# Optimization experiments

Hardware: AMD Instinct MI355X
Metric: run time of the kernel (lower is better)

The kernel has to match this reference:

```python
import jax, jax.numpy as jnp
import numpy as np

B, L, D, H = 2, 2048, 1024, 16
DH = D // H
TAU = 0.1


def setup_inputs() -> dict:
    key = jax.random.key(0)
    ks = jax.random.split(key, 12)
    s = 0.02
    return {
        "q_x": jax.random.normal(ks[0], (B, L, D), jnp.float32),
        "k_x": jax.random.normal(ks[1], (B, L, D), jnp.float32),
        "v_x": jax.random.normal(ks[2], (B, L, D), jnp.float32),
        "ec": jax.random.normal(ks[3], (B, L, D), jnp.float32),
        "Wq": jax.random.normal(ks[4], (D, D), jnp.float32) * s,
        "bq": jnp.zeros((D,), jnp.float32),
        "Wk": jax.random.normal(ks[5], (D, D), jnp.float32) * s,
        "bk": jnp.zeros((D,), jnp.float32),
        "Wv": jax.random.normal(ks[6], (D, D), jnp.float32) * s,
        "bv": jnp.zeros((D,), jnp.float32),
        "Wo": jax.random.normal(ks[7], (D, D), jnp.float32) * s,
        "bo": jnp.zeros((D,), jnp.float32),
    }


def reference(q_x, k_x, v_x, ec, Wq, bq, Wk, bk, Wv, bv, Wo, bo):
    # torch nn.Linear: y = x @ W.T + b
    Q = (q_x @ Wq.T + bq).reshape(B, L, H, DH).transpose(0, 2, 1, 3)   # [B,H,L,Dh]
    K = (k_x @ Wk.T + bk).reshape(B, -1, H, DH).transpose(0, 2, 1, 3)  # [B,H,S,Dh]
    V = (v_x @ Wv.T + bv).reshape(B, -1, H, DH).transpose(0, 2, 1, 3)  # [B,H,S,Dh]
    scores = jnp.einsum("bhld,bhsd->bhls", Q, K) / jnp.sqrt(jnp.float32(DH))
    w = jnp.nan_to_num(jax.nn.softmax(scores, axis=-1), nan=0.0)       # [B,H,L,S]
    # frequency gate per key position: sigmoid((mean|ec| - tau) * 10)
    gate = jax.nn.sigmoid((jnp.abs(ec).mean(-1) - TAU) * 10.0)          # [B,S]
    w = w * gate[:, None, None, :]
    out = jnp.einsum("bhls,bhsd->bhld", w, V)                           # [B,H,L,Dh]
    out = out.transpose(0, 2, 1, 3).reshape(B, L, D)
    return out @ Wo.T + bo
```

## Files before the change

### kernel.cpp

```cpp
#include <hip/hip_runtime.h>

typedef unsigned short u16;
typedef unsigned int u32;
typedef unsigned long long u64;
typedef __attribute__((ext_vector_type(8))) short bf16x8;
typedef __attribute__((ext_vector_type(4))) float f32x4;
typedef __attribute__((ext_vector_type(2))) unsigned int u32x2;
typedef __attribute__((ext_vector_type(4))) unsigned int u32x4;

#define B_ 2
#define L_ 2048
#define D_ 1024
#define H_ 16
#define M_ 4096

__device__ __forceinline__ u16 f2bf(float f) {
  u32 x = __builtin_bit_cast(u32, f);
  return (u16)((x + 0x7fffu + ((x >> 16) & 1u)) >> 16);
}
__device__ __forceinline__ float bf2f(u16 v) {
  return __builtin_bit_cast(float, (u32)v << 16);
}
__device__ __forceinline__ u32 cvtpk(float lo, float hi) {
  u32 r;
  asm("v_cvt_pk_bf16_f32 %0, %1, %2" : "=v"(r) : "v"(lo), "v"(hi));
  return r;
}

__device__ __forceinline__ void lane_regroup(u32& a, u32& b) {
#if __has_builtin(__builtin_amdgcn_permlane32_swap) && \
    __has_builtin(__builtin_amdgcn_permlane16_swap)
  u32x2 r = __builtin_amdgcn_permlane32_swap(a, b, false, false);
  u32x2 t = __builtin_amdgcn_permlane16_swap(r.x, r.y, false, false);
  a = t.x;
  b = t.y;
#else
  asm("v_permlane32_swap_b32 %0, %1\n\t"
      "v_permlane16_swap_b32 %0, %1"
      : "+v"(a), "+v"(b));
#endif
}

__device__ __forceinline__ void gl2lds16(void* lds, const void* g) {
  __builtin_amdgcn_global_load_lds(
      (const __attribute__((address_space(1))) u32*)g,
      (__attribute__((address_space(3))) u32*)lds, 16, 0, 0);
}

__global__ void cvt_all(const float* __restrict__ q, const float* __restrict__ k,
                        const float* __restrict__ v, const float* __restrict__ wq,
                        const float* __restrict__ wk, const float* __restrict__ wv,
                        const float* __restrict__ wo, u16* __restrict__ Xq,
                        u16* __restrict__ Xk, u16* __restrict__ Xv, u16* __restrict__ Wqb,
                        u16* __restrict__ Wkb, u16* __restrict__ Wvb,
                        u16* __restrict__ Wob) {
  int i = blockIdx.x * 256 + threadIdx.x;
  const float* s;
  u16* d;
  int off;
  if (i < 3145728) {
    int t = i >> 20;
    off = i & 1048575;
    s = t == 0 ? q : t == 1 ? k : v;
    d = t == 0 ? Xq : t == 1 ? Xk : Xv;
  } else {
    int j = i - 3145728;
    int t = j >> 18;
    off = j & 262143;
    s = t == 0 ? wq : t == 1 ? wk : t == 2 ? wv : wo;
    d = t == 0 ? Wqb : t == 1 ? Wkb : t == 2 ? Wvb : Wob;
  }
  float4 vv = ((const float4*)s)[off];
  ((u64*)d)[off] = (u64)cvtpk(vv.x, vv.y) | ((u64)cvtpk(vv.z, vv.w) << 32);
}

__global__ void gate_kernel(const float* __restrict__ ec, float* __restrict__ gate) {
  int row = blockIdx.x * 4 + (threadIdx.x >> 6);
  int lane = threadIdx.x & 63;
  const float4* p = (const float4*)(ec + (size_t)row * 1024);
  float s = 0.f;
#pragma unroll
  for (int i = 0; i < 4; i++) {
    float4 v = p[i * 64 + lane];
    s += fabsf(v.x) + fabsf(v.y) + fabsf(v.z) + fabsf(v.w);
  }
#pragma unroll
  for (int m = 1; m < 64; m <<= 1) s += __shfl_xor(s, m);
  if (lane == 0) {
    float mean = s * (1.0f / 1024.0f);
    gate[row] = 1.0f / (1.0f + __expf(-(mean - 0.1f) * 10.0f));
  }
}

__global__ __launch_bounds__(256, 2) void gemm_qkv(
    const u16* __restrict__ Xq, const u16* __restrict__ Xk, const u16* __restrict__ Xv,
    const u16* __restrict__ Wq, const u16* __restrict__ Wk, const u16* __restrict__ Wv,
    const float* __restrict__ bq, const float* __restrict__ bk,
    const float* __restrict__ bv, u16* __restrict__ Qo, u16* __restrict__ Ko,
    u16* __restrict__ Vo) {
  __shared__ u16 As[128 * 64];
  __shared__ u16 Bs[128 * 64];
  const int which = blockIdx.x >> 8;
  const u16* A = which == 0 ? Xq : which == 1 ? Xk : Xv;
  const u16* Bw = which == 0 ? Wq : which == 1 ? Wk : Wv;
  const float* bias = which == 0 ? bq : which == 1 ? bk : bv;
  u16* Cout = which == 0 ? Qo : which == 1 ? Ko : Vo;
  const int bi = blockIdx.x & 255;
  const int K = 1024, N = 1024;
  const int tid = threadIdx.x;
  const int tm = bi >> 3;
  const int tn = bi & 7;
  const int w = tid >> 6, lane = tid & 63;
  const int c = lane & 15, g = lane >> 4;
  const int wr = (w >> 1) << 6, wc = (w & 1) << 6;

  f32x4 acc[4][4] = {};
  const int srow = tid >> 3;
  const int sch = tid & 7;

  for (int kb = 0; kb < K; kb += 64) {
#pragma unroll
    for (int i = 0; i < 4; i++) {
      int row = i * 32 + srow;
      int chs = (sch ^ (row & 7)) << 3;
      gl2lds16((char*)As + i * 4096 + w * 1024,
               A + (size_t)(tm * 128 + row) * K + kb + chs);
      gl2lds16((char*)Bs + i * 4096 + w * 1024,
               Bw + (size_t)(tn * 128 + row) * K + kb + chs);
    }
    __syncthreads();
#pragma unroll
    for (int kd = 0; kd < 2; kd++) {
      bf16x8 af[4], bfr[4];
#pragma unroll
      for (int fi = 0; fi < 4; fi++) {
        int ra = wr + fi * 16 + c;
        af[fi] = *(const bf16x8*)((const char*)As + ra * 128 +
                                  ((((kd << 2) | g) ^ (ra & 7)) << 4));
        int rb = wc + fi * 16 + c;
        bfr[fi] = *(const bf16x8*)((const char*)Bs + rb * 128 +
                                   ((((kd << 2) | g) ^ (rb & 7)) << 4));
      }
#pragma unroll
      for (int fi = 0; fi < 4; fi++)
#pragma unroll
        for (int fj = 0; fj < 4; fj++)
          acc[fi][fj] = __builtin_amdgcn_mfma_f32_16x16x32_bf16(af[fi], bfr[fj],
                                                                acc[fi][fj], 0, 0, 0);
    }
    __syncthreads();
  }

  const int rowb = tm * 128 + wr + g * 4;
  const int colb = tn * 128 + wc + c;
#pragma unroll
  for (int fj = 0; fj < 4; fj++) {
    int col = colb + fj * 16;
    float bv2 = bias[col];
#pragma unroll
    for (int fi = 0; fi < 4; fi++) {
      int r0 = rowb + fi * 16;
#pragma unroll
      for (int r = 0; r < 4; r++)
        Cout[(size_t)(r0 + r) * N + col] = f2bf(acc[fi][fj][r] + bv2);
    }
  }
}

__global__ __launch_bounds__(256, 2) void gemm_o(const u16* __restrict__ A,
                                                 const u16* __restrict__ Bw,
                                                 const float* __restrict__ bias,
                                                 float* __restrict__ Cout) {
  __shared__ u16 As[128 * 64];
  __shared__ u16 Bs[128 * 64];
  const int K = 1024, N = 1024;
  const int tid = threadIdx.x;
  const int tm = blockIdx.x >> 3;
  const int tn = blockIdx.x & 7;
  const int w = tid >> 6, lane = tid & 63;
  const int c = lane & 15, g = lane >> 4;
  const int wr = (w >> 1) << 6, wc = (w & 1) << 6;

  f32x4 acc[4][4] = {};
  const int srow = tid >> 3;
  const int sch = tid & 7;

  for (int kb = 0; kb < K; kb += 64) {
#pragma unroll
    for (int i = 0; i < 4; i++) {
      int row = i * 32 + srow;
      int chs = (sch ^ (row & 7)) << 3;
      gl2lds16((char*)As + i * 4096 + w * 1024,
               A + (size_t)(tm * 128 + row) * K + kb + chs);
      gl2lds16((char*)Bs + i * 4096 + w * 1024,
               Bw + (size_t)(tn * 128 + row) * K + kb + chs);
    }
    __syncthreads();
#pragma unroll
    for (int kd = 0; kd < 2; kd++) {
      bf16x8 af[4], bfr[4];
#pragma unroll
      for (int fi = 0; fi < 4; fi++) {
        int ra = wr + fi * 16 + c;
        af[fi] = *(const bf16x8*)((const char*)As + ra * 128 +
                                  ((((kd << 2) | g) ^ (ra & 7)) << 4));
        int rb = wc + fi * 16 + c;
        bfr[fi] = *(const bf16x8*)((const char*)Bs + rb * 128 +
                                   ((((kd << 2) | g) ^ (rb & 7)) << 4));
      }
#pragma unroll
      for (int fi = 0; fi < 4; fi++)
#pragma unroll
        for (int fj = 0; fj < 4; fj++)
          acc[fi][fj] = __builtin_amdgcn_mfma_f32_16x16x32_bf16(af[fi], bfr[fj],
                                                                acc[fi][fj], 0, 0, 0);
    }
    __syncthreads();
  }

  const int rowb = tm * 128 + wr + g * 4;
  const int colb = tn * 128 + wc + c;
#pragma unroll
  for (int fj = 0; fj < 4; fj++) {
    int col = colb + fj * 16;
    float bv2 = bias[col];
#pragma unroll
    for (int fi = 0; fi < 4; fi++) {
      int r0 = rowb + fi * 16;
#pragma unroll
      for (int r = 0; r < 4; r++)
        Cout[(size_t)(r0 + r) * N + col] = acc[fi][fj][r] + bv2;
    }
  }
}

__global__ void vtrans_kernel(const u16* __restrict__ V, const float* __restrict__ gate,
                              u16* __restrict__ Vt) {
  __shared__ u16 T[64][136];
  const int bh = blockIdx.x >> 4;
  const int stile = blockIdx.x & 15;
  const int b = bh >> 4, h = bh & 15;
  const int tid = threadIdx.x;
  const int sbase = stile * 128;
  const int sl = tid >> 4, dq = tid & 15;
#pragma unroll
  for (int p = 0; p < 8; p++) {
    int s = p * 16 + sl;
    float gg = gate[b * L_ + sbase + s];
    u64 v = *(const u64*)(V + (size_t)(b * L_ + sbase + s) * D_ + h * 64 + dq * 4);
    T[dq * 4 + 0][s] = f2bf(bf2f((u16)(v)) * gg);
    T[dq * 4 + 1][s] = f2bf(bf2f((u16)(v >> 16)) * gg);
    T[dq * 4 + 2][s] = f2bf(bf2f((u16)(v >> 32)) * gg);
    T[dq * 4 + 3][s] = f2bf(bf2f((u16)(v >> 48)) * gg);
  }
  __syncthreads();
  const int d = tid >> 2;
#pragma unroll
  for (int p = 0; p < 4; p++) {
    int ch = p * 4 + (tid & 3);
    bf16x8 vv = *(const bf16x8*)((const char*)T + d * 272 + ch * 16);
    *(bf16x8*)(Vt + (size_t)(bh * 64 + d) * 2048 + sbase + ch * 8) = vv;
  }
}

__global__ __launch_bounds__(256, 3) void attn_kernel(const u16* __restrict__ Qb,
                                                      const u16* __restrict__ Kb,
                                                      const u16* __restrict__ Vt,
                                                      u16* __restrict__ Ob) {
  __shared__ u16 Ks[128 * 64];
  __shared__ u16 Vs[64 * 128];
  const int bi = blockIdx.x;
  const int bh = (bi & 7) | ((bi >> 7) << 3);
  const int qt = (bi >> 3) & 15;
  const int b = bh >> 4, h = bh & 15;
  const int tid = threadIdx.x, w = tid >> 6, lane = tid & 63;
  const int c = lane & 15, g = lane >> 4;
  const int qrow0 = b * L_ + qt * 128 + w * 32;
  const float SCL = 0.18033688011112042f;

  bf16x8 qf[2][2];
#pragma unroll
  for (int fj = 0; fj < 2; fj++)
#pragma unroll
    for (int kd = 0; kd < 2; kd++)
      qf[fj][kd] = *(const bf16x8*)(Qb + (size_t)(qrow0 + fj * 16 + c) * D_ + h * 64 +
                                    kd * 32 + g * 8);

  float lsum[2] = {0.f, 0.f};
  f32x4 oacc[4][2] = {};

  const int srow = tid >> 3, sch = tid & 7;
  const int vrow = tid >> 4, vch = tid & 15;

  for (int kv = 0; kv < 16; kv++) {
    int sbase = kv * 128;
#pragma unroll
    for (int i = 0; i < 4; i++) {
      int kr = i * 32 + srow;
      gl2lds16((char*)Ks + i * 4096 + w * 1024,
               Kb + (size_t)(b * L_ + sbase + kr) * D_ + h * 64 + ((sch ^ (kr & 7)) << 3));
      int vr = i * 16 + vrow;
      gl2lds16((char*)Vs + i * 4096 + w * 1024,
               Vt + (size_t)(bh * 64 + vr) * 2048 + sbase + ((vch ^ (vr & 15)) << 3));
    }
    __syncthreads();

#pragma unroll
    for (int fj = 0; fj < 2; fj++) {
      f32x4 st[8] = {};
#pragma unroll
      for (int kd = 0; kd < 2; kd++) {
#pragma unroll
        for (int fi = 0; fi < 8; fi++) {
          int row = fi * 16 + c;
          bf16x8 kf = *(const bf16x8*)((const char*)Ks + row * 128 +
                                       ((((kd << 2) | g) ^ (c & 7)) << 4));
          st[fi] = __builtin_amdgcn_mfma_f32_16x16x32_bf16(kf, qf[fj][kd], st[fi], 0, 0, 0);
        }
      }
      float rs = 0.f;
      u32 pkA[8], pkB[8];
#pragma unroll
      for (int fi = 0; fi < 8; fi++) {
        float p0 = __builtin_amdgcn_exp2f(st[fi][0] * SCL);
        float p1 = __builtin_amdgcn_exp2f(st[fi][1] * SCL);
        float p2 = __builtin_amdgcn_exp2f(st[fi][2] * SCL);
        float p3 = __builtin_amdgcn_exp2f(st[fi][3] * SCL);
        rs += (p0 + p1) + (p2 + p3);
        pkA[fi] = cvtpk(p0, p1);
        pkB[fi] = cvtpk(p2, p3);
      }
      rs += __shfl_xor(rs, 16);
      rs += __shfl_xor(rs, 32);
      lsum[fj] += rs;
#pragma unroll
      for (int ks = 0; ks < 4; ks++) {
        u32 a0 = pkA[2 * ks], b0 = pkA[2 * ks + 1];
        lane_regroup(a0, b0);
        u32 a1 = pkB[2 * ks], b1 = pkB[2 * ks + 1];
        lane_regroup(a1, b1);
        u32x4 pw = {a0, a1, b0, b1};
        bf16x8 pf = __builtin_bit_cast(bf16x8, pw);
#pragma unroll
        for (int fd = 0; fd < 4; fd++) {
          int vr2 = fd * 16 + c;
          bf16x8 vf = *(const bf16x8*)((const char*)Vs + vr2 * 256 +
                                       ((((ks << 2) | g) ^ (vr2 & 15)) << 4));
          oacc[fd][fj] = __builtin_amdgcn_mfma_f32_16x16x32_bf16(vf, pf, oacc[fd][fj],
                                                                 0, 0, 0);
        }
      }
    }
    __syncthreads();
  }

#pragma unroll
  for (int fj = 0; fj < 2; fj++) {
    float inv = 1.0f / lsum[fj];
    size_t orow = (size_t)(qrow0 + fj * 16 + c) * D_ + h * 64;
#pragma unroll
    for (int fd = 0; fd < 4; fd++) {
      u64 pk = (u64)cvtpk(oacc[fd][fj][0] * inv, oacc[fd][fj][1] * inv) |
               ((u64)cvtpk(oacc[fd][fj][2] * inv, oacc[fd][fj][3] * inv) << 32);
      *(u64*)(Ob + orow + fd * 16 + g * 4) = pk;
    }
  }
}

extern "C" void kernel_launch(void* const* d_in, const int* in_sizes, int n_in,
                              void* d_out, int out_size, void* d_ws, size_t ws_size,
                              hipStream_t stream) {
  const float* q_x = (const float*)d_in[0];
  const float* k_x = (const float*)d_in[1];
  const float* v_x = (const float*)d_in[2];
  const float* ec = (const float*)d_in[3];
  const float* Wq = (const float*)d_in[4];
  const float* bq = (const float*)d_in[5];
  const float* Wk = (const float*)d_in[6];
  const float* bk = (const float*)d_in[7];
  const float* Wv = (const float*)d_in[8];
  const float* bv = (const float*)d_in[9];
  const float* Wo = (const float*)d_in[10];
  const float* bo = (const float*)d_in[11];

  char* ws = (char*)d_ws;
  const size_t MB = 1024 * 1024;
  u16* Wqb = (u16*)(ws + 0 * MB);
  u16* Wkb = (u16*)(ws + 2 * MB);
  u16* Wvb = (u16*)(ws + 4 * MB);
  u16* Wob = (u16*)(ws + 6 * MB);
  float* gatep = (float*)(ws + 8 * MB);
  u16* Xq = (u16*)(ws + 9 * MB);
  u16* Xk = (u16*)(ws + 17 * MB);
  u16* Xv = (u16*)(ws + 25 * MB);
  u16* Qb = (u16*)(ws + 33 * MB);
  u16* Kb = (u16*)(ws + 41 * MB);
  u16* Vb = (u16*)(ws + 49 * MB);
  u16* Vtb = Xq;
  u16* Ab = Xk;

  cvt_all<<<16384, 256, 0, stream>>>(q_x, k_x, v_x, Wq, Wk, Wv, Wo, Xq, Xk, Xv, Wqb,
                                     Wkb, Wvb, Wob);
  gate_kernel<<<1024, 256, 0, stream>>>(ec, gatep);
  gemm_qkv<<<768, 256, 0, stream>>>(Xq, Xk, Xv, Wqb, Wkb, Wvb, bq, bk, bv, Qb, Kb, Vb);
  vtrans_kernel<<<512, 256, 0, stream>>>(Vb, gatep, Vtb);
  attn_kernel<<<512, 256, 0, stream>>>(Qb, Kb, Vtb, Ab);
  gemm_o<<<256, 256, 0, stream>>>(Ab, Wob, bo, (float*)d_out);
}
```

Measured before the change: 141.6 us.

## Double-buffer LDS loads in GEMMs and attention; fuse V transpose+gate into QKV epilogue

Converts the QKV GEMM, output GEMM and attention kernels to a two-stage LDS ping-pong, issuing the next tile's global-to-LDS loads before computing on the current one and waiting with explicit vmcnt counts. The V projection epilogue now applies the gate, transposes through shared memory and writes V^T directly, which removes the separate vtrans kernel and its extra read and write of V. LDS use per block doubles to 64KB, and attention's launch bound drops from 3 to 2 blocks per CU, which may cut occupancy.

```diff
diff --git a/kernel.cpp b/kernel.cpp
--- a/kernel.cpp
+++ b/kernel.cpp
@@ -17,9 +17,6 @@
 __device__ __forceinline__ u16 f2bf(float f) {
   u32 x = __builtin_bit_cast(u32, f);
   return (u16)((x + 0x7fffu + ((x >> 16) & 1u)) >> 16);
-}
-__device__ __forceinline__ float bf2f(u16 v) {
-  return __builtin_bit_cast(float, (u32)v << 16);
 }
 __device__ __forceinline__ u32 cvtpk(float lo, float hi) {
   u32 r;
@@ -45,6 +42,18 @@
   __builtin_amdgcn_global_load_lds(
       (const __attribute__((address_space(1))) u32*)g,
       (__attribute__((address_space(3))) u32*)lds, 16, 0, 0);
+}
+
+__device__ __forceinline__ void wait_vm8() {
+  asm volatile("s_waitcnt vmcnt(8)" ::: "memory");
+}
+__device__ __forceinline__ void wait_vm0() {
+  asm volatile("s_waitcnt vmcnt(0)" ::: "memory");
+}
+__device__ __forceinline__ void bar() {
+  asm volatile("" ::: "memory");
+  __builtin_amdgcn_s_barrier();
+  asm volatile("" ::: "memory");
 }
 
 __global__ void cvt_all(const float* __restrict__ q, const float* __restrict__ k,
@@ -96,50 +105,57 @@
     const u16* __restrict__ Xq, const u16* __restrict__ Xk, const u16* __restrict__ Xv,
     const u16* __restrict__ Wq, const u16* __restrict__ Wk, const u16* __restrict__ Wv,
     const float* __restrict__ bq, const float* __restrict__ bk,
-    const float* __restrict__ bv, u16* __restrict__ Qo, u16* __restrict__ Ko,
-    u16* __restrict__ Vo) {
-  __shared__ u16 As[128 * 64];
-  __shared__ u16 Bs[128 * 64];
+    const float* __restrict__ bv, const float* __restrict__ gate,
+    u16* __restrict__ Qo, u16* __restrict__ Ko, u16* __restrict__ Vt) {
+  __shared__ char smem[65536];
   const int which = blockIdx.x >> 8;
   const u16* A = which == 0 ? Xq : which == 1 ? Xk : Xv;
   const u16* Bw = which == 0 ? Wq : which == 1 ? Wk : Wv;
   const float* bias = which == 0 ? bq : which == 1 ? bk : bv;
-  u16* Cout = which == 0 ? Qo : which == 1 ? Ko : Vo;
   const int bi = blockIdx.x & 255;
-  const int K = 1024, N = 1024;
   const int tid = threadIdx.x;
   const int tm = bi >> 3;
   const int tn = bi & 7;
   const int w = tid >> 6, lane = tid & 63;
   const int c = lane & 15, g = lane >> 4;
   const int wr = (w >> 1) << 6, wc = (w & 1) << 6;
+  const int srow = tid >> 3, sch = tid & 7;
 
   f32x4 acc[4][4] = {};
-  const int srow = tid >> 3;
-  const int sch = tid & 7;
-
-  for (int kb = 0; kb < K; kb += 64) {
+
+  auto stage = [&](int buf, int t) {
+    char* As = smem + buf * 32768;
+    char* Bs = As + 16384;
 #pragma unroll
     for (int i = 0; i < 4; i++) {
       int row = i * 32 + srow;
       int chs = (sch ^ (row & 7)) << 3;
-      gl2lds16((char*)As + i * 4096 + w * 1024,
-               A + (size_t)(tm * 128 + row) * K + kb + chs);
-      gl2lds16((char*)Bs + i * 4096 + w * 1024,
-               Bw + (size_t)(tn * 128 + row) * K + kb + chs);
-    }
-    __syncthreads();
+      gl2lds16(As + i * 4096 + w * 1024, A + (size_t)(tm * 128 + row) * 1024 + t * 64 + chs);
+      gl2lds16(Bs + i * 4096 + w * 1024, Bw + (size_t)(tn * 128 + row) * 1024 + t * 64 + chs);
+    }
+  };
+
+  stage(0, 0);
+  for (int t = 0; t < 16; t++) {
+    int cur = t & 1;
+    if (t < 15) {
+      stage(cur ^ 1, t + 1);
+      wait_vm8();
+    } else {
+      wait_vm0();
+    }
+    bar();
+    const char* As = smem + cur * 32768;
+    const char* Bs = As + 16384;
 #pragma unroll
     for (int kd = 0; kd < 2; kd++) {
       bf16x8 af[4], bfr[4];
 #pragma unroll
       for (int fi = 0; fi < 4; fi++) {
         int ra = wr + fi * 16 + c;
-        af[fi] = *(const bf16x8*)((const char*)As + ra * 128 +
-                                  ((((kd << 2) | g) ^ (ra & 7)) << 4));
+        af[fi] = *(const bf16x8*)(As + ra * 128 + ((((kd << 2) | g) ^ (ra & 7)) << 4));
         int rb = wc + fi * 16 + c;
-        bfr[fi] = *(const bf16x8*)((const char*)Bs + rb * 128 +
-                                   ((((kd << 2) | g) ^ (rb & 7)) << 4));
+        bfr[fi] = *(const bf16x8*)(Bs + rb * 128 + ((((kd << 2) | g) ^ (rb & 7)) << 4));
       }
 #pragma unroll
       for (int fi = 0; fi < 4; fi++)
@@ -148,21 +164,50 @@
           acc[fi][fj] = __builtin_amdgcn_mfma_f32_16x16x32_bf16(af[fi], bfr[fj],
                                                                 acc[fi][fj], 0, 0, 0);
     }
+    bar();
+  }
+
+  if (which == 2) {
+    u16* T = (u16*)smem;
     __syncthreads();
-  }
-
-  const int rowb = tm * 128 + wr + g * 4;
-  const int colb = tn * 128 + wc + c;
-#pragma unroll
-  for (int fj = 0; fj < 4; fj++) {
-    int col = colb + fj * 16;
-    float bv2 = bias[col];
 #pragma unroll
     for (int fi = 0; fi < 4; fi++) {
-      int r0 = rowb + fi * 16;
-#pragma unroll
-      for (int r = 0; r < 4; r++)
-        Cout[(size_t)(r0 + r) * N + col] = f2bf(acc[fi][fj][r] + bv2);
+      int lr0 = wr + fi * 16 + g * 4;
+      float4 gg = *(const float4*)(gate + tm * 128 + lr0);
+#pragma unroll
+      for (int fj = 0; fj < 4; fj++) {
+        int lc = wc + fj * 16 + c;
+        float bv2 = bias[tn * 128 + lc];
+        T[lc * 136 + lr0 + 0] = f2bf((acc[fi][fj][0] + bv2) * gg.x);
+        T[lc * 136 + lr0 + 1] = f2bf((acc[fi][fj][1] + bv2) * gg.y);
+        T[lc * 136 + lr0 + 2] = f2bf((acc[fi][fj][2] + bv2) * gg.z);
+        T[lc * 136 + lr0 + 3] = f2bf((acc[fi][fj][3] + bv2) * gg.w);
+      }
+    }
+    __syncthreads();
+    const int lc = tid >> 1, hf = tid & 1;
+    const int vtrow = (tm >> 4) * 1024 + tn * 128 + lc;
+    const int s0 = (tm & 15) * 128 + hf * 64;
+    const char* Trow = (const char*)(T + lc * 136) + hf * 128;
+    u16* dst = Vt + (size_t)vtrow * 2048 + s0;
+#pragma unroll
+    for (int j = 0; j < 8; j++)
+      *(bf16x8*)(dst + j * 8) = *(const bf16x8*)(Trow + j * 16);
+  } else {
+    u16* Cout = which == 0 ? Qo : Ko;
+    const int rowb = tm * 128 + wr + g * 4;
+    const int colb = tn * 128 + wc + c;
+#pragma unroll
+    for (int fj = 0; fj < 4; fj++) {
+      int col = colb + fj * 16;
+      float bv2 = bias[col];
+#pragma unroll
+      for (int fi = 0; fi < 4; fi++) {
+        int r0 = rowb + fi * 16;
+#pragma unroll
+        for (int r = 0; r < 4; r++)
+          Cout[(size_t)(r0 + r) * 1024 + col] = f2bf(acc[fi][fj][r] + bv2);
+      }
     }
   }
 }
@@ -171,42 +216,50 @@
                                                  const u16* __restrict__ Bw,
                                                  const float* __restrict__ bias,
                                                  float* __restrict__ Cout) {
-  __shared__ u16 As[128 * 64];
-  __shared__ u16 Bs[128 * 64];
-  const int K = 1024, N = 1024;
+  __shared__ char smem[65536];
   const int tid = threadIdx.x;
   const int tm = blockIdx.x >> 3;
   const int tn = blockIdx.x & 7;
   const int w = tid >> 6, lane = tid & 63;
   const int c = lane & 15, g = lane >> 4;
   const int wr = (w >> 1) << 6, wc = (w & 1) << 6;
+  const int srow = tid >> 3, sch = tid & 7;
 
   f32x4 acc[4][4] = {};
-  const int srow = tid >> 3;
-  const int sch = tid & 7;
-
-  for (int kb = 0; kb < K; kb += 64) {
+
+  auto stage = [&](int buf, int t) {
+    char* As = smem + buf * 32768;
+    char* Bs = As + 16384;
 #pragma unroll
     for (int i = 0; i < 4; i++) {
       int row = i * 32 + srow;
       int chs = (sch ^ (row & 7)) << 3;
-      gl2lds16((char*)As + i * 4096 + w * 1024,
-               A + (size_t)(tm * 128 + row) * K + kb + chs);
-      gl2lds16((char*)Bs + i * 4096 + w * 1024,
-               Bw + (size_t)(tn * 128 + row) * K + kb + chs);
-    }
-    __syncthreads();
+      gl2lds16(As + i * 4096 + w * 1024, A + (size_t)(tm * 128 + row) * 1024 + t * 64 + chs);
+      gl2lds16(Bs + i * 4096 + w * 1024, Bw + (size_t)(tn * 128 + row) * 1024 + t * 64 + chs);
+    }
+  };
+
+  stage(0, 0);
+  for (int t = 0; t < 16; t++) {
+    int cur = t & 1;
+    if (t < 15) {
+      stage(cur ^ 1, t + 1);
+      wait_vm8();
+    } else {
+      wait_vm0();
+    }
+    bar();
+    const char* As = smem + cur * 32768;
+    const char* Bs = As + 16384;
 #pragma unroll
     for (int kd = 0; kd < 2; kd++) {
       bf16x8 af[4], bfr[4];
 #pragma unroll
       for (int fi = 0; fi < 4; fi++) {
         int ra = wr + fi * 16 + c;
-        af[fi] = *(const bf16x8*)((const char*)As + ra * 128 +
-                                  ((((kd << 2) | g) ^ (ra & 7)) << 4));
+        af[fi] = *(const bf16x8*)(As + ra * 128 + ((((kd << 2) | g) ^ (ra & 7)) << 4));
         int rb = wc + fi * 16 + c;
-        bfr[fi] = *(const bf16x8*)((const char*)Bs + rb * 128 +
-                                   ((((kd << 2) | g) ^ (rb & 7)) << 4));
+        bfr[fi] = *(const bf16x8*)(Bs + rb * 128 + ((((kd << 2) | g) ^ (rb & 7)) << 4));
       }
 #pragma unroll
       for (int fi = 0; fi < 4; fi++)
@@ -215,7 +268,7 @@
           acc[fi][fj] = __builtin_amdgcn_mfma_f32_16x16x32_bf16(af[fi], bfr[fj],
                                                                 acc[fi][fj], 0, 0, 0);
     }
-    __syncthreads();
+    bar();
   }
 
   const int rowb = tm * 128 + wr + g * 4;
@@ -229,46 +282,16 @@
       int r0 = rowb + fi * 16;
 #pragma unroll
       for (int r = 0; r < 4; r++)
-        Cout[(size_t)(r0 + r) * N + col] = acc[fi][fj][r] + bv2;
-    }
-  }
-}
-
-__global__ void vtrans_kernel(const u16* __restrict__ V, const float* __restrict__ gate,
-                              u16* __restrict__ Vt) {
-  __shared__ u16 T[64][136];
-  const int bh = blockIdx.x >> 4;
-  const int stile = blockIdx.x & 15;
-  const int b = bh >> 4, h = bh & 15;
-  const int tid = threadIdx.x;
-  const int sbase = stile * 128;
-  const int sl = tid >> 4, dq = tid & 15;
-#pragma unroll
-  for (int p = 0; p < 8; p++) {
-    int s = p * 16 + sl;
-    float gg = gate[b * L_ + sbase + s];
-    u64 v = *(const u64*)(V + (size_t)(b * L_ + sbase + s) * D_ + h * 64 + dq * 4);
-    T[dq * 4 + 0][s] = f2bf(bf2f((u16)(v)) * gg);
-    T[dq * 4 + 1][s] = f2bf(bf2f((u16)(v >> 16)) * gg);
-    T[dq * 4 + 2][s] = f2bf(bf2f((u16)(v >> 32)) * gg);
-    T[dq * 4 + 3][s] = f2bf(bf2f((u16)(v >> 48)) * gg);
-  }
-  __syncthreads();
-  const int d = tid >> 2;
-#pragma unroll
-  for (int p = 0; p < 4; p++) {
-    int ch = p * 4 + (tid & 3);
-    bf16x8 vv = *(const bf16x8*)((const char*)T + d * 272 + ch * 16);
-    *(bf16x8*)(Vt + (size_t)(bh * 64 + d) * 2048 + sbase + ch * 8) = vv;
-  }
-}
-
-__global__ __launch_bounds__(256, 3) void attn_kernel(const u16* __restrict__ Qb,
+        Cout[(size_t)(r0 + r) * 1024 + col] = acc[fi][fj][r] + bv2;
+    }
+  }
+}
+
+__global__ __launch_bounds__(256, 2) void attn_kernel(const u16* __restrict__ Qb,
                                                       const u16* __restrict__ Kb,
                                                       const u16* __restrict__ Vt,
                                                       u16* __restrict__ Ob) {
-  __shared__ u16 Ks[128 * 64];
-  __shared__ u16 Vs[64 * 128];
+  __shared__ char asmem[65536];
   const int bi = blockIdx.x;
   const int bh = (bi & 7) | ((bi >> 7) << 3);
   const int qt = (bi >> 3) & 15;
@@ -292,18 +315,33 @@
   const int srow = tid >> 3, sch = tid & 7;
   const int vrow = tid >> 4, vch = tid & 15;
 
-  for (int kv = 0; kv < 16; kv++) {
+  auto stage = [&](int buf, int kv) {
+    char* KsB = asmem + buf * 32768;
+    char* VsB = KsB + 16384;
     int sbase = kv * 128;
 #pragma unroll
     for (int i = 0; i < 4; i++) {
       int kr = i * 32 + srow;
-      gl2lds16((char*)Ks + i * 4096 + w * 1024,
+      gl2lds16(KsB + i * 4096 + w * 1024,
                Kb + (size_t)(b * L_ + sbase + kr) * D_ + h * 64 + ((sch ^ (kr & 7)) << 3));
       int vr = i * 16 + vrow;
-      gl2lds16((char*)Vs + i * 4096 + w * 1024,
+      gl2lds16(VsB + i * 4096 + w * 1024,
                Vt + (size_t)(bh * 64 + vr) * 2048 + sbase + ((vch ^ (vr & 15)) << 3));
     }
-    __syncthreads();
+  };
+
+  stage(0, 0);
+  for (int kv = 0; kv < 16; kv++) {
+    int cur = kv & 1;
+    if (kv < 15) {
+      stage(cur ^ 1, kv + 1);
+      wait_vm8();
+    } else {
+      wait_vm0();
+    }
+    bar();
+    const char* Ks = asmem + cur * 32768;
+    const char* Vs = Ks + 16384;
 
 #pragma unroll
     for (int fj = 0; fj < 2; fj++) {
@@ -313,8 +351,7 @@
 #pragma unroll
         for (int fi = 0; fi < 8; fi++) {
           int row = fi * 16 + c;
-          bf16x8 kf = *(const bf16x8*)((const char*)Ks + row * 128 +
-                                       ((((kd << 2) | g) ^ (c & 7)) << 4));
+          bf16x8 kf = *(const bf16x8*)(Ks + row * 128 + ((((kd << 2) | g) ^ (c & 7)) << 4));
           st[fi] = __builtin_amdgcn_mfma_f32_16x16x32_bf16(kf, qf[fj][kd], st[fi], 0, 0, 0);
         }
       }
@@ -344,14 +381,13 @@
 #pragma unroll
         for (int fd = 0; fd < 4; fd++) {
           int vr2 = fd * 16 + c;
-          bf16x8 vf = *(const bf16x8*)((const char*)Vs + vr2 * 256 +
-                                       ((((ks << 2) | g) ^ (vr2 & 15)) << 4));
+          bf16x8 vf = *(const bf16x8*)(Vs + vr2 * 256 + ((((ks << 2) | g) ^ (vr2 & 15)) << 4));
           oacc[fd][fj] = __builtin_amdgcn_mfma_f32_16x16x32_bf16(vf, pf, oacc[fd][fj],
                                                                  0, 0, 0);
         }
       }
     }
-    __syncthreads();
+    bar();
   }
 
 #pragma unroll
@@ -395,15 +431,14 @@
   u16* Xv = (u16*)(ws + 25 * MB);
   u16* Qb = (u16*)(ws + 33 * MB);
   u16* Kb = (u16*)(ws + 41 * MB);
-  u16* Vb = (u16*)(ws + 49 * MB);
-  u16* Vtb = Xq;
+  u16* Vtb = (u16*)(ws + 49 * MB);
   u16* Ab = Xk;
 
+  gate_kernel<<<1024, 256, 0, stream>>>(ec, gatep);
   cvt_all<<<16384, 256, 0, stream>>>(q_x, k_x, v_x, Wq, Wk, Wv, Wo, Xq, Xk, Xv, Wqb,
                                      Wkb, Wvb, Wob);
-  gate_kernel<<<1024, 256, 0, stream>>>(ec, gatep);
-  gemm_qkv<<<768, 256, 0, stream>>>(Xq, Xk, Xv, Wqb, Wkb, Wvb, bq, bk, bv, Qb, Kb, Vb);
-  vtrans_kernel<<<512, 256, 0, stream>>>(Vb, gatep, Vtb);
+  gemm_qkv<<<768, 256, 0, stream>>>(Xq, Xk, Xv, Wqb, Wkb, Wvb, bq, bk, bv, gatep, Qb,
+                                    Kb, Vtb);
   attn_kernel<<<512, 256, 0, stream>>>(Qb, Kb, Vtb, Ab);
   gemm_o<<<256, 256, 0, stream>>>(Ab, Wob, bo, (float*)d_out);
 }
```

Result: faster. 120.2 us (-15.1%).
